# Kernel tuning notes

Hardware: AMD Instinct MI355X
Metric: run time of the kernel (lower is better)

The kernel has to match this reference:

```python
import jax, jax.numpy as jnp
import numpy as np
from jax import lax

C = 32   # hidden channels (hardcoded in ConvGRUCell.forward)
WID = 7  # spatial width (hardcoded)
A = 8    # num_actions
T = 64
N = 128
H = C * WID * WID  # 1568
DN = ('NCHW', 'OIHW', 'NCHW')


def _conv(x, W, b):
    y = lax.conv_general_dilated(x, W, (1, 1), 'SAME', dimension_numbers=DN)
    return y + b[None, :, None, None]


def _gate(x, W1, b1, W2, b2):
    # Conv -> ReLU -> Conv (matches nn.Sequential in ConvGRUCell)
    return _conv(jax.nn.relu(_conv(x, W1, b1)), W2, b2)


def setup_inputs() -> dict:
    key = jax.random.key(0)
    ks = jax.random.split(key, 18)
    s = 0.1  # weight scale
    act_idx = jax.random.randint(ks[4], (T, N), 0, A)
    return {
        'x': jax.random.normal(ks[0], (T * N, H), jnp.float32),
        'hxs': jax.random.normal(ks[1], (N, H), jnp.float32),
        'attention': jax.random.uniform(ks[2], (T * N, H), jnp.float32),
        'masks': (jax.random.uniform(ks[3], (T * N, 1)) > 0.1).astype(jnp.float32),
        'prev_action_one_hot': jax.nn.one_hot(act_idx, A, dtype=jnp.float32),
        'Wr1': s * jax.random.normal(ks[5], (C, A + C, 3, 3), jnp.float32),
        'br1': jnp.zeros((C,), jnp.float32),
        'Wr2': s * jax.random.normal(ks[6], (C, C, 3, 3), jnp.float32),
        'br2': jnp.zeros((C,), jnp.float32),
        'Wu1': s * jax.random.normal(ks[7], (C, A + C, 3, 3), jnp.float32),
        'bu1': jnp.zeros((C,), jnp.float32),
        'Wu2': s * jax.random.normal(ks[8], (C, C, 3, 3), jnp.float32),
        'bu2': jnp.zeros((C,), jnp.float32),
        'Wo1': s * jax.random.normal(ks[9], (C, A + C, 3, 3), jnp.float32),
        'bo1': jnp.zeros((C,), jnp.float32),
        'Wo2': s * jax.random.normal(ks[10], (C, C, 3, 3), jnp.float32),
        'bo2': jnp.zeros((C,), jnp.float32),
    }


def reference(x, hxs, attention, masks, prev_action_one_hot,
              Wr1, br1, Wr2, br2, Wu1, bu1, Wu2, bu2, Wo1, bo1, Wo2, bo2):
    n = hxs.shape[0]
    t = x.shape[0] // n
    xs = x.reshape(t, n, H)
    ms = masks.reshape(t, n, 1)
    att = attention.reshape(t, n, H)

    def step(h, inputs):
        xi, mi, ai, pai = inputs
        hidden = h * mi + xi * (1.0 - mi)          # [N, H]
        prev = hidden.reshape(n, C, WID, WID)
        inp = (pai * mi)[:, :, None, None]          # [N, A, 1, 1]
        inp = jnp.broadcast_to(inp, (n, A, WID, WID))
        stacked = jnp.concatenate([inp, prev], axis=1)  # [N, A+C, 7, 7]
        update = jax.nn.sigmoid(_gate(stacked, Wu1, bu1, Wu2, bu2))
        reset = jax.nn.sigmoid(_gate(stacked, Wr1, br1, Wr2, br2))
        out_in = jnp.tanh(_gate(jnp.concatenate([inp, prev * reset], axis=1),
                                Wo1, bo1, Wo2, bo2))
        p_mu = (prev * (1.0 - update) + out_in * update).reshape(n, H)
        attended = xi * ai + p_mu * (1.0 - ai)      # new hxs
        return attended, (p_mu, attended)

    hxs_f, (p_mu, attended) = lax.scan(step, hxs, (xs, ms, att, prev_action_one_hot))
    return p_mu.reshape(t * n, H), attended.reshape(t * n, H), hxs_f
```

## Files before the change

kernel.cpp:

```cpp
#include <hip/hip_runtime.h>
#include <math.h>


#define TT 64
#define NB 128
#define CC 32
#define AA 8
#define SS 49
#define HH 1568
#define KK 288
#define NKB 9
#define NPOS 81
#define NTHR 512

typedef short bf16x8 __attribute__((ext_vector_type(8)));
typedef short bf16x4 __attribute__((ext_vector_type(4)));
typedef float f32x4 __attribute__((ext_vector_type(4)));

struct __align__(16) SMEM {
  union {
    short staging[CC * KK];
    struct {
      short stacked[NPOS * CC];
      short img_u[NPOS * CC];
      short img_r[NPOS * CC];
    } im;
  } u;
  short wsum[3 * 9 * CC * AA];
  short cArr[3 * 9 * CC];
  float sH[HH];
  float sU[HH];
  float sO[HH];
  float bias[6 * CC];
};

__device__ __forceinline__ short f2bf(float v) {
  union { float f; unsigned u; } a; a.f = v;
  unsigned r = a.u + 0x7FFFu + ((a.u >> 16) & 1u);
  return (short)(r >> 16);
}
__device__ __forceinline__ float b2f(short h) {
  union { unsigned u; float f; } a; a.u = ((unsigned)(unsigned short)h) << 16;
  return a.f;
}
__device__ __forceinline__ float sigm(float v) { return 1.f / (1.f + __expf(-v)); }
__device__ __forceinline__ float tanhfast(float v) { return 2.f / (1.f + __expf(-2.f * v)) - 1.f; }

__device__ __forceinline__ int swz(int p, int ci) {
  return ((p << 5) + ci) ^ (((p >> 1) & 3) << 3);
}
__device__ __forceinline__ int clsOf(int s) {
  int y = s / 7, x = s - y * 7;
  return (y == 0 ? 0 : (y == 6 ? 6 : 3)) + (x == 0 ? 0 : (x == 6 ? 2 : 1));
}

__device__ __forceinline__ f32x4 conv288(const short* img, const bf16x8 (&fA)[NKB],
                                         const int (&ad)[NKB])
{
  f32x4 a0 = {0.f, 0.f, 0.f, 0.f}, a1 = {0.f, 0.f, 0.f, 0.f};
#pragma unroll
  for (int b = 0; b < NKB; b += 2) {
    a0 = __builtin_amdgcn_mfma_f32_16x16x32_bf16(fA[b], *(const bf16x8*)(img + ad[b]), a0, 0, 0, 0);
    if (b + 1 < NKB)
      a1 = __builtin_amdgcn_mfma_f32_16x16x32_bf16(fA[b + 1], *(const bf16x8*)(img + ad[b + 1]), a1, 0, 0, 0);
  }
  return a0 + a1;
}

__global__ __launch_bounds__(NTHR, 2)
void convgru_mfma(const float* __restrict__ x, const float* __restrict__ hxs,
                  const float* __restrict__ att, const float* __restrict__ masks,
                  const float* __restrict__ pact,
                  const float* __restrict__ Wr1, const float* __restrict__ br1,
                  const float* __restrict__ Wr2, const float* __restrict__ br2,
                  const float* __restrict__ Wu1, const float* __restrict__ bu1,
                  const float* __restrict__ Wu2, const float* __restrict__ bu2,
                  const float* __restrict__ Wo1, const float* __restrict__ bo1,
                  const float* __restrict__ Wo2, const float* __restrict__ bo2,
                  float* __restrict__ out)
{
  __shared__ SMEM sm;
  const int n = blockIdx.x;
  const int tid = threadIdx.x;
  const int w = __builtin_amdgcn_readfirstlane(tid >> 6);
  const int lane = tid & 63;
  const int gate = w >> 2;
  const int wq = w & 3;
  const int mt = w & 1;
  const int sbase = (wq >> 1) * 2;
  const int stO = w >> 1;
  const int fg = lane >> 4;
  const int col = lane & 15;
  const int co0 = mt * 16 + fg * 4;

  if (tid < 6 * CC) {
    const float* bsrc[6] = {bu1, bu2, br1, br2, bo1, bo2};
    sm.bias[tid] = bsrc[tid >> 5][tid & 31];
  }

  bf16x8 fG1[NKB], fG2[NKB], fO1[NKB], fO2[NKB];
  {
    const float* wsrc[6] = {Wu1, Wr1, Wo1, Wu2, Wr2, Wo2};
    const int fco = mt * 16 + col;
#pragma unroll
    for (int cv = 0; cv < 6; ++cv) {
      __syncthreads();
      const float* wp = wsrc[cv];
      const int cin = (cv < 3) ? (AA + CC) : CC;
      const int cofs = (cv < 3) ? AA : 0;
      for (int i = tid; i < CC * KK; i += NTHR) {
        int co = i / KK, k = i - co * KK;
        int tap = k >> 5, pc = k & 31;
        sm.u.staging[(co * KK + k) ^ ((co & 7) << 3)] =
            f2bf(wp[(co * cin + cofs + pc) * 9 + tap]);
      }
      __syncthreads();
      auto loadfr = [&](bf16x8 (&dst)[NKB]) {
#pragma unroll
        for (int b = 0; b < NKB; ++b)
          dst[b] = *(const bf16x8*)&sm.u.staging[(fco * KK + b * 32 + fg * 8) ^ ((fco & 7) << 3)];
      };
      if (cv == 0) { if (gate == 0) loadfr(fG1); }
      else if (cv == 1) { if (gate == 1) loadfr(fG1); }
      else if (cv == 2) { loadfr(fO1); }
      else if (cv == 3) { if (gate == 0) loadfr(fG2); }
      else if (cv == 4) { if (gate == 1) loadfr(fG2); }
      else { loadfr(fO2); }
    }
  }
  __syncthreads();

  for (int i = tid; i < CC * KK; i += NTHR) sm.u.staging[i] = 0;
  {
    const float* w1s[3] = {Wu1, Wr1, Wo1};
    for (int e = tid; e < 3 * 9 * CC * AA; e += NTHR) {
      int g = e / 2304, rem = e - g * 2304;
      int cls = rem >> 8;
      int co = (rem >> 3) & 31, ci = e & 7;
      int yt = cls / 3, xt = cls - yt * 3;
      const float* wp = w1s[g] + (co * (AA + CC) + ci) * 9;
      float s = 0.f;
#pragma unroll
      for (int r = 0; r < 3; ++r) {
        if ((yt == 0 && r == 0) || (yt == 2 && r == 2)) continue;
#pragma unroll
        for (int c = 0; c < 3; ++c) {
          if ((xt == 0 && c == 0) || (xt == 2 && c == 2)) continue;
          s += wp[r * 3 + c];
        }
      }
      sm.wsum[e] = f2bf(s);
    }
  }

  int sg[2], pout_sw[2], clsAG[2], inG[2][NKB]; bool vG[2];
#pragma unroll
  for (int j = 0; j < 2; ++j) {
    int s = (sbase + j) * 16 + col;
    vG[j] = (s < SS); int sc = vG[j] ? s : (SS - 1); sg[j] = sc;
    int y = sc / 7, xx = sc - y * 7;
    int p0 = y * 9 + xx;
    pout_sw[j] = swz(p0 + 10, co0);
    clsAG[j] = ((gate * 9 + clsOf(sc)) << 5) + co0;
#pragma unroll
    for (int b = 0; b < NKB; ++b)
      inG[j][b] = swz(p0 + (b / 3) * 9 + (b % 3), fg * 8);
  }
  int sOv, pout_swO, clsAO, inO[NKB]; bool vO;
  {
    int s = stO * 16 + col;
    vO = (s < SS); int sc = vO ? s : (SS - 1); sOv = sc;
    int y = sc / 7, xx = sc - y * 7;
    int p0 = y * 9 + xx;
    pout_swO = swz(p0 + 10, co0);
    clsAO = ((2 * 9 + clsOf(sc)) << 5) + co0;
#pragma unroll
    for (int b = 0; b < NKB; ++b)
      inO[b] = swz(p0 + (b / 3) * 9 + (b % 3), fg * 8);
  }

  int eidx[4], stSw[4]; bool eval[4];
#pragma unroll
  for (int j = 0; j < 4; ++j) {
    int i = tid + j * NTHR;
    eval[j] = (i < HH);
    int ii = eval[j] ? i : 0;
    eidx[j] = ii;
    int co = ii / SS, s = ii - co * SS;
    int y = s / 7, xx = s - y * 7;
    stSw[j] = swz(y * 9 + xx + 10, co);
  }

  float* out_pmu = out;
  float* out_att = out + (size_t)TT * NB * HH;
  float* out_h   = out + (size_t)2 * TT * NB * HH;

  __syncthreads();

  f32x4 biaG2, biaO2;
#pragma unroll
  for (int q = 0; q < 4; ++q) {
    biaG2[q] = sm.bias[(gate * 2 + 1) * 32 + co0 + q];
    biaO2[q] = sm.bias[5 * 32 + co0 + q];
  }

  auto carr = [&](const float (&v)[8]) {
    for (int e = tid; e < 3 * 9 * CC; e += NTHR) {
      const bf16x8 wv = *(const bf16x8*)&sm.wsum[e << 3];
      int g = e / (9 * CC);
      int co = e & 31;
      float acc = sm.bias[(g << 6) + co];
#pragma unroll
      for (int q = 0; q < 8; ++q) acc = fmaf(b2f(wv[q]), v[q], acc);
      sm.cArr[e] = f2bf(acc);
    }
  };

  float xcar[4];
  {
    const float m0 = masks[n];
    const float* x0 = x + (size_t)n * HH;
    const float* h0 = hxs + (size_t)n * HH;
#pragma unroll
    for (int j = 0; j < 4; ++j) if (eval[j]) {
      float xv = x0[eidx[j]];
      float h = h0[eidx[j]] * m0 + xv * (1.f - m0);
      sm.sH[eidx[j]] = h;
      sm.u.im.stacked[stSw[j]] = f2bf(h);
      xcar[j] = xv;
    }
    float v0[8];
    const float* pa0 = pact + (size_t)n * AA;
#pragma unroll
    for (int q = 0; q < 8; ++q) v0[q] = pa0[q] * m0;
    carr(v0);
  }
  __syncthreads();

  for (int t = 0; t < TT; ++t) {
    const bool last = (t == TT - 1);
    const size_t obase = ((size_t)(t * NB) + n) * HH;

    const float* atp = att + obase;
    const int tn = last ? t : (t + 1);
    const float* xnp = x + ((size_t)(tn * NB) + n) * HH;
    float xnv[4], avv[4];
#pragma unroll
    for (int j = 0; j < 4; ++j) { avv[j] = atp[eidx[j]]; xnv[j] = xnp[eidx[j]]; }
    const float m2 = last ? 0.f : masks[(t + 1) * NB + n];
    float vN[8];
    const float* pap = pact + ((size_t)(tn * NB) + n) * AA;
#pragma unroll
    for (int q = 0; q < 8; ++q) vN[q] = pap[q] * m2;

    {
      short* imgOut = gate ? sm.u.im.img_r : sm.u.im.img_u;
#pragma unroll
      for (int j = 0; j < 2; ++j) {
        f32x4 a = conv288(sm.u.im.stacked, fG1, inG[j]);
        if (vG[j]) {
          bf16x4 c4 = *(const bf16x4*)&sm.cArr[clsAG[j]];
          bf16x4 pk;
#pragma unroll
          for (int q = 0; q < 4; ++q) pk[q] = f2bf(fmaxf(a[q] + b2f(c4[q]), 0.f));
          *(bf16x4*)&imgOut[pout_sw[j]] = pk;
        }
      }
    }
    __syncthreads();

    if (gate == 0) {
#pragma unroll
      for (int j = 0; j < 2; ++j) {
        f32x4 a = conv288(sm.u.im.img_u, fG2, inG[j]);
        if (vG[j]) {
#pragma unroll
          for (int q = 0; q < 4; ++q)
            sm.sU[(co0 + q) * SS + sg[j]] = sigm(a[q] + biaG2[q]);
        }
      }
    } else {
#pragma unroll
      for (int j = 0; j < 2; ++j) {
        f32x4 a = conv288(sm.u.im.img_r, fG2, inG[j]);
        if (vG[j]) {
          bf16x4 pk;
#pragma unroll
          for (int q = 0; q < 4; ++q) {
            float rv = sigm(a[q] + biaG2[q]);
            pk[q] = f2bf(sm.sH[(co0 + q) * SS + sg[j]] * rv);
          }
          *(bf16x4*)&sm.u.im.stacked[pout_sw[j]] = pk;
        }
      }
    }
    __syncthreads();

    {
      f32x4 a = conv288(sm.u.im.stacked, fO1, inO);
      if (vO) {
        bf16x4 c4 = *(const bf16x4*)&sm.cArr[clsAO];
        bf16x4 pk;
#pragma unroll
        for (int q = 0; q < 4; ++q) pk[q] = f2bf(fmaxf(a[q] + b2f(c4[q]), 0.f));
        *(bf16x4*)&sm.u.im.img_u[pout_swO] = pk;
      }
    }
    __syncthreads();

    {
      f32x4 a = conv288(sm.u.im.img_u, fO2, inO);
      if (vO) {
#pragma unroll
        for (int q = 0; q < 4; ++q)
          sm.sO[(co0 + q) * SS + sOv] = tanhfast(a[q] + biaO2[q]);
      }
      if (!last) carr(vN);
    }
    __syncthreads();

    {
#pragma unroll
      for (int j = 0; j < 4; ++j) if (eval[j]) {
        const int ii = eidx[j];
        float uv = sm.sU[ii], ov = sm.sO[ii], pv = sm.sH[ii];
        float pm = pv + (ov - pv) * uv;
        out_pmu[obase + ii] = pm;
        float a = avv[j];
        float at2 = pm + (xcar[j] - pm) * a;
        out_att[obase + ii] = at2;
        if (last) {
          out_h[(size_t)n * HH + ii] = at2;
        } else {
          float h = xnv[j] + (at2 - xnv[j]) * m2;
          sm.sH[ii] = h;
          sm.u.im.stacked[stSw[j]] = f2bf(h);
          xcar[j] = xnv[j];
        }
      }
    }
    __syncthreads();
  }
}

extern "C" void kernel_launch(void* const* d_in, const int* in_sizes, int n_in,
                              void* d_out, int out_size, void* d_ws, size_t ws_size,
                              hipStream_t stream)
{
  const float* x    = (const float*)d_in[0];
  const float* hxs  = (const float*)d_in[1];
  const float* att  = (const float*)d_in[2];
  const float* mks  = (const float*)d_in[3];
  const float* pact = (const float*)d_in[4];
  const float* Wr1  = (const float*)d_in[5];
  const float* br1  = (const float*)d_in[6];
  const float* Wr2  = (const float*)d_in[7];
  const float* br2  = (const float*)d_in[8];
  const float* Wu1  = (const float*)d_in[9];
  const float* bu1  = (const float*)d_in[10];
  const float* Wu2  = (const float*)d_in[11];
  const float* bu2  = (const float*)d_in[12];
  const float* Wo1  = (const float*)d_in[13];
  const float* bo1  = (const float*)d_in[14];
  const float* Wo2  = (const float*)d_in[15];
  const float* bo2  = (const float*)d_in[16];

  convgru_mfma<<<dim3(NB), dim3(NTHR), 0, stream>>>(
      x, hxs, att, mks, pact,
      Wr1, br1, Wr2, br2, Wu1, bu1, Wu2, bu2, Wo1, bo1, Wo2, bo2,
      (float*)d_out);
}
```

Baseline: 272.7 us.

## Specialize wave roles per gate conv and overlap carry computation with output conv

Each pair of waves now gets a fixed role instead of all waves sharing every conv stage. Role 0 computes the update and reset first-layer convs together, reusing one set of loaded B fragments. Roles 1 and 2 run the second-layer update and reset convs. Role 3 runs both output-gate convs while the other waves compute the next step's action carry term from weights held in registers. The aim is fewer redundant LDS fragment loads and overlap of the carry work, but each stage's MFMA work now lands on fewer waves, which can lengthen the serial critical path of every timestep.

```diff
diff --git a/kernel.cpp b/kernel.cpp
--- a/kernel.cpp
+++ b/kernel.cpp
@@ -54,18 +54,7 @@
   return (y == 0 ? 0 : (y == 6 ? 6 : 3)) + (x == 0 ? 0 : (x == 6 ? 2 : 1));
 }
 
-__device__ __forceinline__ f32x4 conv288(const short* img, const bf16x8 (&fA)[NKB],
-                                         const int (&ad)[NKB])
-{
-  f32x4 a0 = {0.f, 0.f, 0.f, 0.f}, a1 = {0.f, 0.f, 0.f, 0.f};
-#pragma unroll
-  for (int b = 0; b < NKB; b += 2) {
-    a0 = __builtin_amdgcn_mfma_f32_16x16x32_bf16(fA[b], *(const bf16x8*)(img + ad[b]), a0, 0, 0, 0);
-    if (b + 1 < NKB)
-      a1 = __builtin_amdgcn_mfma_f32_16x16x32_bf16(fA[b + 1], *(const bf16x8*)(img + ad[b + 1]), a1, 0, 0, 0);
-  }
-  return a0 + a1;
-}
+#define MFMA(A, B, C) __builtin_amdgcn_mfma_f32_16x16x32_bf16((A), (B), (C), 0, 0, 0)
 
 __global__ __launch_bounds__(NTHR, 2)
 void convgru_mfma(const float* __restrict__ x, const float* __restrict__ hxs,
@@ -84,24 +73,19 @@
   const int tid = threadIdx.x;
   const int w = __builtin_amdgcn_readfirstlane(tid >> 6);
   const int lane = tid & 63;
-  const int gate = w >> 2;
-  const int wq = w & 3;
-  const int mt = w & 1;
-  const int sbase = (wq >> 1) * 2;
-  const int stO = w >> 1;
+  const int role = w >> 1;
+  const int b2 = w & 1;
   const int fg = lane >> 4;
   const int col = lane & 15;
-  const int co0 = mt * 16 + fg * 4;
 
   if (tid < 6 * CC) {
     const float* bsrc[6] = {bu1, bu2, br1, br2, bo1, bo2};
     sm.bias[tid] = bsrc[tid >> 5][tid & 31];
   }
 
-  bf16x8 fG1[NKB], fG2[NKB], fO1[NKB], fO2[NKB];
+  bf16x8 fA[4][NKB];
   {
     const float* wsrc[6] = {Wu1, Wr1, Wo1, Wu2, Wr2, Wo2};
-    const int fco = mt * 16 + col;
 #pragma unroll
     for (int cv = 0; cv < 6; ++cv) {
       __syncthreads();
@@ -115,17 +99,18 @@
             f2bf(wp[(co * cin + cofs + pc) * 9 + tap]);
       }
       __syncthreads();
-      auto loadfr = [&](bf16x8 (&dst)[NKB]) {
+      auto loadfr = [&](bf16x8 (&dst)[NKB], int mt) {
+        const int fco = mt * 16 + col;
 #pragma unroll
         for (int b = 0; b < NKB; ++b)
           dst[b] = *(const bf16x8*)&sm.u.staging[(fco * KK + b * 32 + fg * 8) ^ ((fco & 7) << 3)];
       };
-      if (cv == 0) { if (gate == 0) loadfr(fG1); }
-      else if (cv == 1) { if (gate == 1) loadfr(fG1); }
-      else if (cv == 2) { loadfr(fO1); }
-      else if (cv == 3) { if (gate == 0) loadfr(fG2); }
-      else if (cv == 4) { if (gate == 1) loadfr(fG2); }
-      else { loadfr(fO2); }
+      if (cv == 0 && role == 0) { loadfr(fA[0], 0); loadfr(fA[1], 1); }
+      if (cv == 1 && role == 0) { loadfr(fA[2], 0); loadfr(fA[3], 1); }
+      if (cv == 2 && role == 3) { loadfr(fA[0], 0); loadfr(fA[1], 1); }
+      if (cv == 3 && role == 1) { loadfr(fA[0], 0); loadfr(fA[1], 1); }
+      if (cv == 4 && role == 2) { loadfr(fA[0], 0); loadfr(fA[1], 1); }
+      if (cv == 5 && role == 3) { loadfr(fA[2], 0); loadfr(fA[3], 1); }
     }
   }
   __syncthreads();
@@ -153,30 +138,20 @@
     }
   }
 
-  int sg[2], pout_sw[2], clsAG[2], inG[2][NKB]; bool vG[2];
+  int sg[2], clsJ[2], inJ[2][NKB], poutJ[2][2]; bool vJ[2];
 #pragma unroll
   for (int j = 0; j < 2; ++j) {
-    int s = (sbase + j) * 16 + col;
-    vG[j] = (s < SS); int sc = vG[j] ? s : (SS - 1); sg[j] = sc;
+    int s = (b2 * 2 + j) * 16 + col;
+    vJ[j] = (s < SS); int sc = vJ[j] ? s : (SS - 1); sg[j] = sc;
     int y = sc / 7, xx = sc - y * 7;
     int p0 = y * 9 + xx;
-    pout_sw[j] = swz(p0 + 10, co0);
-    clsAG[j] = ((gate * 9 + clsOf(sc)) << 5) + co0;
+    clsJ[j] = clsOf(sc);
+#pragma unroll
+    for (int mt = 0; mt < 2; ++mt)
+      poutJ[j][mt] = swz(p0 + 10, mt * 16 + fg * 4);
 #pragma unroll
     for (int b = 0; b < NKB; ++b)
-      inG[j][b] = swz(p0 + (b / 3) * 9 + (b % 3), fg * 8);
-  }
-  int sOv, pout_swO, clsAO, inO[NKB]; bool vO;
-  {
-    int s = stO * 16 + col;
-    vO = (s < SS); int sc = vO ? s : (SS - 1); sOv = sc;
-    int y = sc / 7, xx = sc - y * 7;
-    int p0 = y * 9 + xx;
-    pout_swO = swz(p0 + 10, co0);
-    clsAO = ((2 * 9 + clsOf(sc)) << 5) + co0;
-#pragma unroll
-    for (int b = 0; b < NKB; ++b)
-      inO[b] = swz(p0 + (b / 3) * 9 + (b % 3), fg * 8);
+      inJ[j][b] = swz(p0 + (b / 3) * 9 + (b % 3), fg * 8);
   }
 
   int eidx[4], stSw[4]; bool eval[4];
@@ -197,22 +172,36 @@
 
   __syncthreads();
 
-  f32x4 biaG2, biaO2;
-#pragma unroll
-  for (int q = 0; q < 4; ++q) {
-    biaG2[q] = sm.bias[(gate * 2 + 1) * 32 + co0 + q];
-    biaO2[q] = sm.bias[5 * 32 + co0 + q];
+  f32x4 bia2[2];
+  {
+    const int bb = (role == 2) ? 96 : (role == 3) ? 160 : 32;
+#pragma unroll
+    for (int mt = 0; mt < 2; ++mt)
+#pragma unroll
+      for (int q = 0; q < 4; ++q)
+        bia2[mt][q] = sm.bias[bb + mt * 16 + fg * 4 + q];
+  }
+
+  const bool carrOwn = (tid >= 128 && tid < 384);
+  const int lt = tid - 128;
+  bf16x8 wR[4]; float bR[4]; bool okC[4];
+#pragma unroll
+  for (int k = 0; k < 4; ++k) {
+    int e = lt + 256 * k;
+    okC[k] = carrOwn && (e < 3 * 9 * CC);
+    if (okC[k]) {
+      wR[k] = *(const bf16x8*)&sm.wsum[e << 3];
+      bR[k] = sm.bias[((e / 288) << 6) + (e & 31)];
+    }
   }
 
   auto carr = [&](const float (&v)[8]) {
-    for (int e = tid; e < 3 * 9 * CC; e += NTHR) {
-      const bf16x8 wv = *(const bf16x8*)&sm.wsum[e << 3];
-      int g = e / (9 * CC);
-      int co = e & 31;
-      float acc = sm.bias[(g << 6) + co];
-#pragma unroll
-      for (int q = 0; q < 8; ++q) acc = fmaf(b2f(wv[q]), v[q], acc);
-      sm.cArr[e] = f2bf(acc);
+#pragma unroll
+    for (int k = 0; k < 4; ++k) if (okC[k]) {
+      float acc = bR[k];
+#pragma unroll
+      for (int q = 0; q < 8; ++q) acc = fmaf(b2f(wR[k][q]), v[q], acc);
+      sm.cArr[lt + 256 * k] = f2bf(acc);
     }
   };
 
@@ -253,69 +242,149 @@
 #pragma unroll
     for (int q = 0; q < 8; ++q) vN[q] = pap[q] * m2;
 
-    {
-      short* imgOut = gate ? sm.u.im.img_r : sm.u.im.img_u;
+    if (role == 0) {
 #pragma unroll
       for (int j = 0; j < 2; ++j) {
-        f32x4 a = conv288(sm.u.im.stacked, fG1, inG[j]);
-        if (vG[j]) {
-          bf16x4 c4 = *(const bf16x4*)&sm.cArr[clsAG[j]];
+        bf16x8 bv[NKB];
+#pragma unroll
+        for (int b = 0; b < NKB; ++b)
+          bv[b] = *(const bf16x8*)&sm.u.im.stacked[inJ[j][b]];
+        f32x4 aU0 = {0.f,0.f,0.f,0.f}, aU1 = {0.f,0.f,0.f,0.f};
+        f32x4 aR0 = {0.f,0.f,0.f,0.f}, aR1 = {0.f,0.f,0.f,0.f};
+#pragma unroll
+        for (int b = 0; b < NKB; ++b) {
+          aU0 = MFMA(fA[0][b], bv[b], aU0);
+          aU1 = MFMA(fA[1][b], bv[b], aU1);
+          aR0 = MFMA(fA[2][b], bv[b], aR0);
+          aR1 = MFMA(fA[3][b], bv[b], aR1);
+        }
+        if (vJ[j]) {
+          bf16x4 c4, pk;
+          c4 = *(const bf16x4*)&sm.cArr[(clsJ[j] << 5) + fg * 4];
+#pragma unroll
+          for (int q = 0; q < 4; ++q) pk[q] = f2bf(fmaxf(aU0[q] + b2f(c4[q]), 0.f));
+          *(bf16x4*)&sm.u.im.img_u[poutJ[j][0]] = pk;
+          c4 = *(const bf16x4*)&sm.cArr[(clsJ[j] << 5) + 16 + fg * 4];
+#pragma unroll
+          for (int q = 0; q < 4; ++q) pk[q] = f2bf(fmaxf(aU1[q] + b2f(c4[q]), 0.f));
+          *(bf16x4*)&sm.u.im.img_u[poutJ[j][1]] = pk;
+          c4 = *(const bf16x4*)&sm.cArr[((9 + clsJ[j]) << 5) + fg * 4];
+#pragma unroll
+          for (int q = 0; q < 4; ++q) pk[q] = f2bf(fmaxf(aR0[q] + b2f(c4[q]), 0.f));
+          *(bf16x4*)&sm.u.im.img_r[poutJ[j][0]] = pk;
+          c4 = *(const bf16x4*)&sm.cArr[((9 + clsJ[j]) << 5) + 16 + fg * 4];
+#pragma unroll
+          for (int q = 0; q < 4; ++q) pk[q] = f2bf(fmaxf(aR1[q] + b2f(c4[q]), 0.f));
+          *(bf16x4*)&sm.u.im.img_r[poutJ[j][1]] = pk;
+        }
+      }
+    }
+    __syncthreads();
+
+    if (role == 1) {
+#pragma unroll
+      for (int j = 0; j < 2; ++j) {
+        bf16x8 bv[NKB];
+#pragma unroll
+        for (int b = 0; b < NKB; ++b)
+          bv[b] = *(const bf16x8*)&sm.u.im.img_u[inJ[j][b]];
+        f32x4 a0 = {0.f,0.f,0.f,0.f}, a1 = {0.f,0.f,0.f,0.f};
+#pragma unroll
+        for (int b = 0; b < NKB; ++b) {
+          a0 = MFMA(fA[0][b], bv[b], a0);
+          a1 = MFMA(fA[1][b], bv[b], a1);
+        }
+        if (vJ[j]) {
+#pragma unroll
+          for (int q = 0; q < 4; ++q) {
+            sm.sU[(fg * 4 + q) * SS + sg[j]]      = sigm(a0[q] + bia2[0][q]);
+            sm.sU[(16 + fg * 4 + q) * SS + sg[j]] = sigm(a1[q] + bia2[1][q]);
+          }
+        }
+      }
+    } else if (role == 2) {
+#pragma unroll
+      for (int j = 0; j < 2; ++j) {
+        bf16x8 bv[NKB];
+#pragma unroll
+        for (int b = 0; b < NKB; ++b)
+          bv[b] = *(const bf16x8*)&sm.u.im.img_r[inJ[j][b]];
+        f32x4 a0 = {0.f,0.f,0.f,0.f}, a1 = {0.f,0.f,0.f,0.f};
+#pragma unroll
+        for (int b = 0; b < NKB; ++b) {
+          a0 = MFMA(fA[0][b], bv[b], a0);
+          a1 = MFMA(fA[1][b], bv[b], a1);
+        }
+        if (vJ[j]) {
           bf16x4 pk;
 #pragma unroll
-          for (int q = 0; q < 4; ++q) pk[q] = f2bf(fmaxf(a[q] + b2f(c4[q]), 0.f));
-          *(bf16x4*)&imgOut[pout_sw[j]] = pk;
+          for (int q = 0; q < 4; ++q) {
+            float rv = sigm(a0[q] + bia2[0][q]);
+            pk[q] = f2bf(sm.sH[(fg * 4 + q) * SS + sg[j]] * rv);
+          }
+          *(bf16x4*)&sm.u.im.stacked[poutJ[j][0]] = pk;
+#pragma unroll
+          for (int q = 0; q < 4; ++q) {
+            float rv = sigm(a1[q] + bia2[1][q]);
+            pk[q] = f2bf(sm.sH[(16 + fg * 4 + q) * SS + sg[j]] * rv);
+          }
+          *(bf16x4*)&sm.u.im.stacked[poutJ[j][1]] = pk;
         }
       }
     }
     __syncthreads();
 
-    if (gate == 0) {
+    if (role == 3) {
 #pragma unroll
       for (int j = 0; j < 2; ++j) {
-        f32x4 a = conv288(sm.u.im.img_u, fG2, inG[j]);
-        if (vG[j]) {
-#pragma unroll
-          for (int q = 0; q < 4; ++q)
-            sm.sU[(co0 + q) * SS + sg[j]] = sigm(a[q] + biaG2[q]);
-        }
-      }
-    } else {
+        bf16x8 bv[NKB];
+#pragma unroll
+        for (int b = 0; b < NKB; ++b)
+          bv[b] = *(const bf16x8*)&sm.u.im.stacked[inJ[j][b]];
+        f32x4 a0 = {0.f,0.f,0.f,0.f}, a1 = {0.f,0.f,0.f,0.f};
+#pragma unroll
+        for (int b = 0; b < NKB; ++b) {
+          a0 = MFMA(fA[0][b], bv[b], a0);
+          a1 = MFMA(fA[1][b], bv[b], a1);
+        }
+        if (vJ[j]) {
+          bf16x4 c4, pk;
+          c4 = *(const bf16x4*)&sm.cArr[((18 + clsJ[j]) << 5) + fg * 4];
+#pragma unroll
+          for (int q = 0; q < 4; ++q) pk[q] = f2bf(fmaxf(a0[q] + b2f(c4[q]), 0.f));
+          *(bf16x4*)&sm.u.im.img_u[poutJ[j][0]] = pk;
+          c4 = *(const bf16x4*)&sm.cArr[((18 + clsJ[j]) << 5) + 16 + fg * 4];
+#pragma unroll
+          for (int q = 0; q < 4; ++q) pk[q] = f2bf(fmaxf(a1[q] + b2f(c4[q]), 0.f));
+          *(bf16x4*)&sm.u.im.img_u[poutJ[j][1]] = pk;
+        }
+      }
+    }
+    __syncthreads();
+
+    if (role == 3) {
 #pragma unroll
       for (int j = 0; j < 2; ++j) {
-        f32x4 a = conv288(sm.u.im.img_r, fG2, inG[j]);
-        if (vG[j]) {
-          bf16x4 pk;
+        bf16x8 bv[NKB];
+#pragma unroll
+        for (int b = 0; b < NKB; ++b)
+          bv[b] = *(const bf16x8*)&sm.u.im.img_u[inJ[j][b]];
+        f32x4 a0 = {0.f,0.f,0.f,0.f}, a1 = {0.f,0.f,0.f,0.f};
+#pragma unroll
+        for (int b = 0; b < NKB; ++b) {
+          a0 = MFMA(fA[2][b], bv[b], a0);
+          a1 = MFMA(fA[3][b], bv[b], a1);
+        }
+        if (vJ[j]) {
 #pragma unroll
           for (int q = 0; q < 4; ++q) {
-            float rv = sigm(a[q] + biaG2[q]);
-            pk[q] = f2bf(sm.sH[(co0 + q) * SS + sg[j]] * rv);
+            sm.sO[(fg * 4 + q) * SS + sg[j]]      = tanhfast(a0[q] + bia2[0][q]);
+            sm.sO[(16 + fg * 4 + q) * SS + sg[j]] = tanhfast(a1[q] + bia2[1][q]);
           }
-          *(bf16x4*)&sm.u.im.stacked[pout_sw[j]] = pk;
-        }
-      }
-    }
-    __syncthreads();
-
-    {
-      f32x4 a = conv288(sm.u.im.stacked, fO1, inO);
-      if (vO) {
-        bf16x4 c4 = *(const bf16x4*)&sm.cArr[clsAO];
-        bf16x4 pk;
-#pragma unroll
-        for (int q = 0; q < 4; ++q) pk[q] = f2bf(fmaxf(a[q] + b2f(c4[q]), 0.f));
-        *(bf16x4*)&sm.u.im.img_u[pout_swO] = pk;
-      }
-    }
-    __syncthreads();
-
-    {
-      f32x4 a = conv288(sm.u.im.img_u, fO2, inO);
-      if (vO) {
-#pragma unroll
-        for (int q = 0; q < 4; ++q)
-          sm.sO[(co0 + q) * SS + sOv] = tanhfast(a[q] + biaO2[q]);
-      }
-      if (!last) carr(vN);
+        }
+      }
+    } else if (!last) {
+      carr(vN);
     }
     __syncthreads();
 
```

Result: slower. 498.8 us (+82.9%).

## Remap first gate conv so each wave covers both channel halves, reusing B fragments

Applied to the files above, without the earlier changes.

In the first gate convolution, each wave now owns one spatial tile and both 16-channel output halves. It loads the nine input-image fragments once and feeds them to two MFMA chains, instead of loading them separately for two spatial tiles. The per-step constant-array computation also keeps its weight sums and biases in registers, replacing the strided loop with at most two fixed entries per thread. Together these cut LDS reads and loop overhead, at the cost of holding twice as many first-layer weight fragments in registers. That extra register pressure could hurt occupancy under the 2-blocks-per-CU launch bound.

```diff
diff --git a/kernel.cpp b/kernel.cpp
--- a/kernel.cpp
+++ b/kernel.cpp
@@ -54,15 +54,17 @@
   return (y == 0 ? 0 : (y == 6 ? 6 : 3)) + (x == 0 ? 0 : (x == 6 ? 2 : 1));
 }
 
+#define MFMA(A, B, C) __builtin_amdgcn_mfma_f32_16x16x32_bf16((A), (B), (C), 0, 0, 0)
+
 __device__ __forceinline__ f32x4 conv288(const short* img, const bf16x8 (&fA)[NKB],
                                          const int (&ad)[NKB])
 {
   f32x4 a0 = {0.f, 0.f, 0.f, 0.f}, a1 = {0.f, 0.f, 0.f, 0.f};
 #pragma unroll
   for (int b = 0; b < NKB; b += 2) {
-    a0 = __builtin_amdgcn_mfma_f32_16x16x32_bf16(fA[b], *(const bf16x8*)(img + ad[b]), a0, 0, 0, 0);
+    a0 = MFMA(fA[b], *(const bf16x8*)(img + ad[b]), a0);
     if (b + 1 < NKB)
-      a1 = __builtin_amdgcn_mfma_f32_16x16x32_bf16(fA[b + 1], *(const bf16x8*)(img + ad[b + 1]), a1, 0, 0, 0);
+      a1 = MFMA(fA[b + 1], *(const bf16x8*)(img + ad[b + 1]), a1);
   }
   return a0 + a1;
 }
@@ -87,6 +89,7 @@
   const int gate = w >> 2;
   const int wq = w & 3;
   const int mt = w & 1;
+  const int stG = w & 3;
   const int sbase = (wq >> 1) * 2;
   const int stO = w >> 1;
   const int fg = lane >> 4;
@@ -98,10 +101,9 @@
     sm.bias[tid] = bsrc[tid >> 5][tid & 31];
   }
 
-  bf16x8 fG1[NKB], fG2[NKB], fO1[NKB], fO2[NKB];
+  bf16x8 fG1[2][NKB], fG2[NKB], fO1[NKB], fO2[NKB];
   {
     const float* wsrc[6] = {Wu1, Wr1, Wo1, Wu2, Wr2, Wo2};
-    const int fco = mt * 16 + col;
 #pragma unroll
     for (int cv = 0; cv < 6; ++cv) {
       __syncthreads();
@@ -115,17 +117,18 @@
             f2bf(wp[(co * cin + cofs + pc) * 9 + tap]);
       }
       __syncthreads();
-      auto loadfr = [&](bf16x8 (&dst)[NKB]) {
+      auto loadfr = [&](bf16x8 (&dst)[NKB], int m) {
+        const int fco = m * 16 + col;
 #pragma unroll
         for (int b = 0; b < NKB; ++b)
           dst[b] = *(const bf16x8*)&sm.u.staging[(fco * KK + b * 32 + fg * 8) ^ ((fco & 7) << 3)];
       };
-      if (cv == 0) { if (gate == 0) loadfr(fG1); }
-      else if (cv == 1) { if (gate == 1) loadfr(fG1); }
-      else if (cv == 2) { loadfr(fO1); }
-      else if (cv == 3) { if (gate == 0) loadfr(fG2); }
-      else if (cv == 4) { if (gate == 1) loadfr(fG2); }
-      else { loadfr(fO2); }
+      if (cv == 0) { if (gate == 0) { loadfr(fG1[0], 0); loadfr(fG1[1], 1); } }
+      else if (cv == 1) { if (gate == 1) { loadfr(fG1[0], 0); loadfr(fG1[1], 1); } }
+      else if (cv == 2) { loadfr(fO1, mt); }
+      else if (cv == 3) { if (gate == 0) loadfr(fG2, mt); }
+      else if (cv == 4) { if (gate == 1) loadfr(fG2, mt); }
+      else { loadfr(fO2, mt); }
     }
   }
   __syncthreads();
@@ -153,15 +156,29 @@
     }
   }
 
-  int sg[2], pout_sw[2], clsAG[2], inG[2][NKB]; bool vG[2];
+  int in1[NKB], pout1[2], clsA1[2]; bool v1;
+  {
+    int s = stG * 16 + col;
+    v1 = (s < SS); int sc = v1 ? s : (SS - 1);
+    int y = sc / 7, xx = sc - y * 7;
+    int p0 = y * 9 + xx;
+#pragma unroll
+    for (int b = 0; b < NKB; ++b)
+      in1[b] = swz(p0 + (b / 3) * 9 + (b % 3), fg * 8);
+#pragma unroll
+    for (int m = 0; m < 2; ++m) {
+      pout1[m] = swz(p0 + 10, m * 16 + fg * 4);
+      clsA1[m] = ((gate * 9 + clsOf(sc)) << 5) + m * 16 + fg * 4;
+    }
+  }
+  int sg[2], poutG[2], inG[2][NKB]; bool vG[2];
 #pragma unroll
   for (int j = 0; j < 2; ++j) {
     int s = (sbase + j) * 16 + col;
     vG[j] = (s < SS); int sc = vG[j] ? s : (SS - 1); sg[j] = sc;
     int y = sc / 7, xx = sc - y * 7;
     int p0 = y * 9 + xx;
-    pout_sw[j] = swz(p0 + 10, co0);
-    clsAG[j] = ((gate * 9 + clsOf(sc)) << 5) + co0;
+    poutG[j] = swz(p0 + 10, co0);
 #pragma unroll
     for (int b = 0; b < NKB; ++b)
       inG[j][b] = swz(p0 + (b / 3) * 9 + (b % 3), fg * 8);
@@ -204,15 +221,23 @@
     biaO2[q] = sm.bias[5 * 32 + co0 + q];
   }
 
+  const int e1 = tid + NTHR;
+  const bool ok1 = (e1 < 3 * 9 * CC);
+  bf16x8 wR0 = *(const bf16x8*)&sm.wsum[tid << 3];
+  float bR0 = sm.bias[((tid / 288) << 6) + (tid & 31)];
+  bf16x8 wR1 = ok1 ? *(const bf16x8*)&sm.wsum[e1 << 3] : wR0;
+  float bR1 = ok1 ? sm.bias[((e1 / 288) << 6) + (e1 & 31)] : 0.f;
+
   auto carr = [&](const float (&v)[8]) {
-    for (int e = tid; e < 3 * 9 * CC; e += NTHR) {
-      const bf16x8 wv = *(const bf16x8*)&sm.wsum[e << 3];
-      int g = e / (9 * CC);
-      int co = e & 31;
-      float acc = sm.bias[(g << 6) + co];
-#pragma unroll
-      for (int q = 0; q < 8; ++q) acc = fmaf(b2f(wv[q]), v[q], acc);
-      sm.cArr[e] = f2bf(acc);
+    float acc = bR0;
+#pragma unroll
+    for (int q = 0; q < 8; ++q) acc = fmaf(b2f(wR0[q]), v[q], acc);
+    sm.cArr[tid] = f2bf(acc);
+    if (ok1) {
+      float a2 = bR1;
+#pragma unroll
+      for (int q = 0; q < 8; ++q) a2 = fmaf(b2f(wR1[q]), v[q], a2);
+      sm.cArr[e1] = f2bf(a2);
     }
   };
 
@@ -255,15 +280,30 @@
 
     {
       short* imgOut = gate ? sm.u.im.img_r : sm.u.im.img_u;
-#pragma unroll
-      for (int j = 0; j < 2; ++j) {
-        f32x4 a = conv288(sm.u.im.stacked, fG1, inG[j]);
-        if (vG[j]) {
-          bf16x4 c4 = *(const bf16x4*)&sm.cArr[clsAG[j]];
+      bf16x8 bv[NKB];
+#pragma unroll
+      for (int b = 0; b < NKB; ++b)
+        bv[b] = *(const bf16x8*)&sm.u.im.stacked[in1[b]];
+      f32x4 a0m0 = {0.f,0.f,0.f,0.f}, a1m0 = {0.f,0.f,0.f,0.f};
+      f32x4 a0m1 = {0.f,0.f,0.f,0.f}, a1m1 = {0.f,0.f,0.f,0.f};
+#pragma unroll
+      for (int b = 0; b < NKB; b += 2) {
+        a0m0 = MFMA(fG1[0][b], bv[b], a0m0);
+        a0m1 = MFMA(fG1[1][b], bv[b], a0m1);
+        if (b + 1 < NKB) {
+          a1m0 = MFMA(fG1[0][b + 1], bv[b + 1], a1m0);
+          a1m1 = MFMA(fG1[1][b + 1], bv[b + 1], a1m1);
+        }
+      }
+      if (v1) {
+        f32x4 am[2] = {a0m0 + a1m0, a0m1 + a1m1};
+#pragma unroll
+        for (int m = 0; m < 2; ++m) {
+          bf16x4 c4 = *(const bf16x4*)&sm.cArr[clsA1[m]];
           bf16x4 pk;
 #pragma unroll
-          for (int q = 0; q < 4; ++q) pk[q] = f2bf(fmaxf(a[q] + b2f(c4[q]), 0.f));
-          *(bf16x4*)&imgOut[pout_sw[j]] = pk;
+          for (int q = 0; q < 4; ++q) pk[q] = f2bf(fmaxf(am[m][q] + b2f(c4[q]), 0.f));
+          *(bf16x4*)&imgOut[pout1[m]] = pk;
         }
       }
     }
@@ -290,7 +330,7 @@
             float rv = sigm(a[q] + biaG2[q]);
             pk[q] = f2bf(sm.sH[(co0 + q) * SS + sg[j]] * rv);
           }
-          *(bf16x4*)&sm.u.im.stacked[pout_sw[j]] = pk;
+          *(bf16x4*)&sm.u.im.stacked[poutG[j]] = pk;
         }
       }
     }
```

Result: slower. 467.2 us (+71.3%).

## Fuse GRU output epilogue into final conv stage and drop a barrier

Applied to the files above, without the earlier changes.

The per-element GRU combine and output stores move into the epilogue of the last conv (O2), which owns 4 channels by 1 spatial position per lane. This removes the sO shared buffer and one __syncthreads per timestep. Global loads and stores now follow the MFMA output mapping, so they are strided by 49 floats and less coalesced. The cArr weight sums and biases are hoisted into registers instead of being reloaded each step.

```diff
diff --git a/kernel.cpp b/kernel.cpp
--- a/kernel.cpp
+++ b/kernel.cpp
@@ -30,7 +30,6 @@
   short cArr[3 * 9 * CC];
   float sH[HH];
   float sU[HH];
-  float sO[HH];
   float bias[6 * CC];
 };
 
@@ -54,15 +53,17 @@
   return (y == 0 ? 0 : (y == 6 ? 6 : 3)) + (x == 0 ? 0 : (x == 6 ? 2 : 1));
 }
 
+#define MFMA(A, B, C) __builtin_amdgcn_mfma_f32_16x16x32_bf16((A), (B), (C), 0, 0, 0)
+
 __device__ __forceinline__ f32x4 conv288(const short* img, const bf16x8 (&fA)[NKB],
                                          const int (&ad)[NKB])
 {
   f32x4 a0 = {0.f, 0.f, 0.f, 0.f}, a1 = {0.f, 0.f, 0.f, 0.f};
 #pragma unroll
   for (int b = 0; b < NKB; b += 2) {
-    a0 = __builtin_amdgcn_mfma_f32_16x16x32_bf16(fA[b], *(const bf16x8*)(img + ad[b]), a0, 0, 0, 0);
+    a0 = MFMA(fA[b], *(const bf16x8*)(img + ad[b]), a0);
     if (b + 1 < NKB)
-      a1 = __builtin_amdgcn_mfma_f32_16x16x32_bf16(fA[b + 1], *(const bf16x8*)(img + ad[b + 1]), a1, 0, 0, 0);
+      a1 = MFMA(fA[b + 1], *(const bf16x8*)(img + ad[b + 1]), a1);
   }
   return a0 + a1;
 }
@@ -153,20 +154,20 @@
     }
   }
 
-  int sg[2], pout_sw[2], clsAG[2], inG[2][NKB]; bool vG[2];
+  int sg[2], poutG[2], clsAG[2], inG[2][NKB]; bool vG[2];
 #pragma unroll
   for (int j = 0; j < 2; ++j) {
     int s = (sbase + j) * 16 + col;
     vG[j] = (s < SS); int sc = vG[j] ? s : (SS - 1); sg[j] = sc;
     int y = sc / 7, xx = sc - y * 7;
     int p0 = y * 9 + xx;
-    pout_sw[j] = swz(p0 + 10, co0);
+    poutG[j] = swz(p0 + 10, co0);
     clsAG[j] = ((gate * 9 + clsOf(sc)) << 5) + co0;
 #pragma unroll
     for (int b = 0; b < NKB; ++b)
       inG[j][b] = swz(p0 + (b / 3) * 9 + (b % 3), fg * 8);
   }
-  int sOv, pout_swO, clsAO, inO[NKB]; bool vO;
+  int sOv, pout_swO, clsAO, inO[NKB], epiBase, stkBase; bool vO;
   {
     int s = stO * 16 + col;
     vO = (s < SS); int sc = vO ? s : (SS - 1); sOv = sc;
@@ -174,21 +175,11 @@
     int p0 = y * 9 + xx;
     pout_swO = swz(p0 + 10, co0);
     clsAO = ((2 * 9 + clsOf(sc)) << 5) + co0;
+    epiBase = co0 * SS + sOv;
+    stkBase = swz(p0 + 10, co0);
 #pragma unroll
     for (int b = 0; b < NKB; ++b)
       inO[b] = swz(p0 + (b / 3) * 9 + (b % 3), fg * 8);
-  }
-
-  int eidx[4], stSw[4]; bool eval[4];
-#pragma unroll
-  for (int j = 0; j < 4; ++j) {
-    int i = tid + j * NTHR;
-    eval[j] = (i < HH);
-    int ii = eval[j] ? i : 0;
-    eidx[j] = ii;
-    int co = ii / SS, s = ii - co * SS;
-    int y = s / 7, xx = s - y * 7;
-    stSw[j] = swz(y * 9 + xx + 10, co);
   }
 
   float* out_pmu = out;
@@ -204,36 +195,48 @@
     biaO2[q] = sm.bias[5 * 32 + co0 + q];
   }
 
+  const int e1 = tid + NTHR;
+  const bool ok1 = (e1 < 3 * 9 * CC);
+  bf16x8 wR0 = *(const bf16x8*)&sm.wsum[tid << 3];
+  float bR0 = sm.bias[((tid / 288) << 6) + (tid & 31)];
+  bf16x8 wR1 = ok1 ? *(const bf16x8*)&sm.wsum[e1 << 3] : wR0;
+  float bR1 = ok1 ? sm.bias[((e1 / 288) << 6) + (e1 & 31)] : 0.f;
+
   auto carr = [&](const float (&v)[8]) {
-    for (int e = tid; e < 3 * 9 * CC; e += NTHR) {
-      const bf16x8 wv = *(const bf16x8*)&sm.wsum[e << 3];
-      int g = e / (9 * CC);
-      int co = e & 31;
-      float acc = sm.bias[(g << 6) + co];
-#pragma unroll
-      for (int q = 0; q < 8; ++q) acc = fmaf(b2f(wv[q]), v[q], acc);
-      sm.cArr[e] = f2bf(acc);
+    float acc = bR0;
+#pragma unroll
+    for (int q = 0; q < 8; ++q) acc = fmaf(b2f(wR0[q]), v[q], acc);
+    sm.cArr[tid] = f2bf(acc);
+    if (ok1) {
+      float a2 = bR1;
+#pragma unroll
+      for (int q = 0; q < 8; ++q) a2 = fmaf(b2f(wR1[q]), v[q], a2);
+      sm.cArr[e1] = f2bf(a2);
     }
   };
 
-  float xcar[4];
   {
     const float m0 = masks[n];
     const float* x0 = x + (size_t)n * HH;
     const float* h0 = hxs + (size_t)n * HH;
-#pragma unroll
-    for (int j = 0; j < 4; ++j) if (eval[j]) {
-      float xv = x0[eidx[j]];
-      float h = h0[eidx[j]] * m0 + xv * (1.f - m0);
-      sm.sH[eidx[j]] = h;
-      sm.u.im.stacked[stSw[j]] = f2bf(h);
-      xcar[j] = xv;
+    for (int i = tid; i < HH; i += NTHR) {
+      float h = h0[i] * m0 + x0[i] * (1.f - m0);
+      sm.sH[i] = h;
+      int co = i / SS, s = i - co * SS;
+      int y = s / 7, xx = s - y * 7;
+      sm.u.im.stacked[swz(y * 9 + xx + 10, co)] = f2bf(h);
     }
     float v0[8];
     const float* pa0 = pact + (size_t)n * AA;
 #pragma unroll
     for (int q = 0; q < 8; ++q) v0[q] = pa0[q] * m0;
     carr(v0);
+  }
+  float xcar[4];
+  {
+    const float* x0 = x + (size_t)n * HH;
+#pragma unroll
+    for (int q = 0; q < 4; ++q) xcar[q] = x0[epiBase + q * SS];
   }
   __syncthreads();
 
@@ -246,7 +249,10 @@
     const float* xnp = x + ((size_t)(tn * NB) + n) * HH;
     float xnv[4], avv[4];
 #pragma unroll
-    for (int j = 0; j < 4; ++j) { avv[j] = atp[eidx[j]]; xnv[j] = xnp[eidx[j]]; }
+    for (int q = 0; q < 4; ++q) {
+      avv[q] = atp[epiBase + q * SS];
+      xnv[q] = xnp[epiBase + q * SS];
+    }
     const float m2 = last ? 0.f : masks[(t + 1) * NB + n];
     float vN[8];
     const float* pap = pact + ((size_t)(tn * NB) + n) * AA;
@@ -263,7 +269,7 @@
           bf16x4 pk;
 #pragma unroll
           for (int q = 0; q < 4; ++q) pk[q] = f2bf(fmaxf(a[q] + b2f(c4[q]), 0.f));
-          *(bf16x4*)&imgOut[pout_sw[j]] = pk;
+          *(bf16x4*)&imgOut[poutG[j]] = pk;
         }
       }
     }
@@ -290,7 +296,7 @@
             float rv = sigm(a[q] + biaG2[q]);
             pk[q] = f2bf(sm.sH[(co0 + q) * SS + sg[j]] * rv);
           }
-          *(bf16x4*)&sm.u.im.stacked[pout_sw[j]] = pk;
+          *(bf16x4*)&sm.u.im.stacked[poutG[j]] = pk;
         }
       }
     }
@@ -312,32 +318,26 @@
       f32x4 a = conv288(sm.u.im.img_u, fO2, inO);
       if (vO) {
 #pragma unroll
-        for (int q = 0; q < 4; ++q)
-          sm.sO[(co0 + q) * SS + sOv] = tanhfast(a[q] + biaO2[q]);
+        for (int q = 0; q < 4; ++q) {
+          const int ii = epiBase + q * SS;
+          float ov = tanhfast(a[q] + biaO2[q]);
+          float uv = sm.sU[ii];
+          float pv = sm.sH[ii];
+          float pm = pv + (ov - pv) * uv;
+          out_pmu[obase + ii] = pm;
+          float at2 = pm + (xcar[q] - pm) * avv[q];
+          out_att[obase + ii] = at2;
+          if (last) {
+            out_h[(size_t)n * HH + ii] = at2;
+          } else {
+            float h = xnv[q] + (at2 - xnv[q]) * m2;
+            sm.sH[ii] = h;
+            sm.u.im.stacked[stkBase + q] = f2bf(h);
+            xcar[q] = xnv[q];
+          }
+        }
       }
       if (!last) carr(vN);
-    }
-    __syncthreads();
-
-    {
-#pragma unroll
-      for (int j = 0; j < 4; ++j) if (eval[j]) {
-        const int ii = eidx[j];
-        float uv = sm.sU[ii], ov = sm.sO[ii], pv = sm.sH[ii];
-        float pm = pv + (ov - pv) * uv;
-        out_pmu[obase + ii] = pm;
-        float a = avv[j];
-        float at2 = pm + (xcar[j] - pm) * a;
-        out_att[obase + ii] = at2;
-        if (last) {
-          out_h[(size_t)n * HH + ii] = at2;
-        } else {
-          float h = xnv[j] + (at2 - xnv[j]) * m2;
-          sm.sH[ii] = h;
-          sm.u.im.stacked[stSw[j]] = f2bf(h);
-          xcar[j] = xnv[j];
-        }
-      }
     }
     __syncthreads();
   }
```

Result: faster. 244.5 us (-10.4%).
